# Optimization experiments

Measured on AMD Instinct MI355X. Metric: run time of the kernel, lower is better.

## Reference

```python
import jax, jax.numpy as jnp
import numpy as np

TEMPERATURE = 0.07
EPS = 1e-12


def setup_inputs() -> dict:
    key = jax.random.key(0)
    k1, k2 = jax.random.split(key)
    B, D = 16384, 256
    return {
        "query_embeds": jax.random.normal(k1, (B, D), dtype=jnp.float32),
        "database_embeds": jax.random.normal(k2, (B, D), dtype=jnp.float32),
    }


def _l2_normalize(x, axis=1):
    # torch F.normalize: x / max(||x||, eps)
    norm = jnp.sqrt(jnp.sum(x * x, axis=axis, keepdims=True))
    return x / jnp.maximum(norm, EPS)


def reference(query_embeds, database_embeds):
    q = _l2_normalize(query_embeds, axis=1)   # [B, D]
    d = _l2_normalize(database_embeds, axis=1)  # [B, D]
    sim = jnp.einsum("bd,cd->bc", q, d) / TEMPERATURE  # [B, B]
    B = sim.shape[0]
    diag = jnp.diagonal(sim)  # logits at the correct (matching) label
    # CE over rows (q->d): -log_softmax(sim, axis=1)[i, i]
    lse_rows = jax.nn.logsumexp(sim, axis=1)
    loss_q2d = jnp.mean(lse_rows - diag)
    # CE over rows of sim.T == columns of sim (d->q)
    lse_cols = jax.nn.logsumexp(sim, axis=0)
    loss_d2q = jnp.mean(lse_cols - diag)
    return (loss_q2d + loss_d2q) / 2
```

## Files before the change

kernel.cpp:

```cpp
#include <hip/hip_runtime.h>
#include <hip/hip_bf16.h>
#include <cstdint>
#include <cstddef>

#define B_ROWS 16384
#define D_DIM  256
#define TEMP_INV 14.285714285714286f

#define NITER 16

using frag_cd = __attribute__((ext_vector_type(4))) float;
using i32x4   = __attribute__((ext_vector_type(4))) int;
using i32x8   = __attribute__((ext_vector_type(8))) int;


__global__ __launch_bounds__(256) void norm_diag_kernel(
    const float* __restrict__ q, const float* __restrict__ d,
    unsigned int* __restrict__ qn, unsigned int* __restrict__ dn,
    float* __restrict__ diag,
    float* __restrict__ row_sums, float* __restrict__ col_sums,
    float* __restrict__ out) {
    const int b = blockIdx.x;
    if (b < 64)            row_sums[b * 256 + threadIdx.x] = 0.0f;
    else if (b < 128)      col_sums[(b - 64) * 256 + threadIdx.x] = 0.0f;
    else if (b == 128 && threadIdx.x == 0) out[0] = 0.0f;

    const int t    = threadIdx.x;
    const int lane = t & 63;
    const int w    = t >> 6;
    const int l15  = lane & 15;
    const int rw   = lane >> 4;
    const int r    = w * 4 + rw;
    const int row  = b * 16 + r;

    const float4* qr = (const float4*)(q + (size_t)row * D_DIM);
    const float4* dr = (const float4*)(d + (size_t)row * D_DIM);
    float4 qv[4], dv[4];
    float qss = 0.f, dss = 0.f, qd = 0.f;
#pragma unroll
    for (int p = 0; p < 4; ++p) {
        qv[p] = qr[l15 + 16 * p];
        dv[p] = dr[l15 + 16 * p];
        qss += qv[p].x*qv[p].x + qv[p].y*qv[p].y + qv[p].z*qv[p].z + qv[p].w*qv[p].w;
        dss += dv[p].x*dv[p].x + dv[p].y*dv[p].y + dv[p].z*dv[p].z + dv[p].w*dv[p].w;
        qd  += qv[p].x*dv[p].x + qv[p].y*dv[p].y + qv[p].z*dv[p].z + qv[p].w*dv[p].w;
    }
#pragma unroll
    for (int off = 1; off < 16; off <<= 1) {
        qss += __shfl_xor(qss, off);
        dss += __shfl_xor(dss, off);
        qd  += __shfl_xor(qd,  off);
    }
    const float qinv = 1.0f / fmaxf(sqrtf(qss), 1e-12f);
    const float dinv = 1.0f / fmaxf(sqrtf(dss), 1e-12f);

    __shared__ unsigned int qbuf[1024], dbuf[1024];
#pragma unroll
    for (int p = 0; p < 4; ++p) {
        const int jw = l15 + 16 * p;
        int qp = 0, dp = 0;
        qp = __builtin_amdgcn_cvt_pk_fp8_f32(qv[p].x * qinv, qv[p].y * qinv, qp, false);
        qp = __builtin_amdgcn_cvt_pk_fp8_f32(qv[p].z * qinv, qv[p].w * qinv, qp, true);
        dp = __builtin_amdgcn_cvt_pk_fp8_f32(dv[p].x * dinv, dv[p].y * dinv, dp, false);
        dp = __builtin_amdgcn_cvt_pk_fp8_f32(dv[p].z * dinv, dv[p].w * dinv, dp, true);
        const int c    = (jw & 31) >> 2;
        const int widx = ((jw >> 5) << 9) | ((c >> 2) << 8) | ((c & 3) << 6)
                       | (r << 2) | (jw & 3);
        qbuf[widx] = (unsigned int)qp;
        dbuf[widx] = (unsigned int)dp;
    }
    if (l15 == 0) diag[row] = qd * qinv * dinv * TEMP_INV;
    __syncthreads();
    ((uint4*)qn)[(size_t)b * 256 + t] = ((const uint4*)qbuf)[t];
    ((uint4*)dn)[(size_t)b * 256 + t] = ((const uint4*)dbuf)[t];
}

__global__ __launch_bounds__(256, 2) void gemm_lse_kernel(
    const unsigned char* __restrict__ qn, const unsigned char* __restrict__ dn,
    float* __restrict__ row_sums, float* __restrict__ col_sums) {
    const int t    = threadIdx.x;
    const int lane = t & 63;
    const int w    = t >> 6;
    const int l15  = lane & 15;
    const int quad = lane >> 4;

    const int id   = blockIdx.x;
    const int xcd  = id & 7;
    const int i    = id >> 3;
    const int chunk   = (xcd << 1) | (i & 1);
    const int rowg    = i >> 1;
    const int rowBase = rowg * 256;
    const int colChunkBase = chunk * 1024;

    union OpU { i32x8 v; i32x4 h[2]; };

    const unsigned char* aB = qn + ((size_t)((rowBase >> 4) + w * 4) << 12) + lane * 16;
    OpU a8[4][2];
#pragma unroll
    for (int mi = 0; mi < 4; ++mi)
#pragma unroll
        for (int kt = 0; kt < 2; ++kt) {
            a8[mi][kt].h[0] = *(const i32x4*)(aB + mi * 4096 + kt * 2048);
            a8[mi][kt].h[1] = *(const i32x4*)(aB + mi * 4096 + kt * 2048 + 1024);
        }

    const unsigned char* bBase = dn + ((size_t)(colChunkBase >> 4) << 12) + lane * 16;

    OpU bC[4], bN[4];
#pragma unroll
    for (int ni = 0; ni < 4; ++ni) {
        bC[ni].h[0] = *(const i32x4*)(bBase + ni * 4096);
        bC[ni].h[1] = *(const i32x4*)(bBase + ni * 4096 + 1024);
    }

    union RV { frag_cd v[4]; float f[16]; } rvu;
#pragma unroll
    for (int k = 0; k < 4; ++k) rvu.v[k] = (frag_cd){0.f, 0.f, 0.f, 0.f};

    const float C2 = TEMP_INV * 1.44269504088896f;

    for (int it = 0; it < NITER; ++it) {
        const unsigned char* bI = bBase + (size_t)it * 16384;

#pragma unroll
        for (int ni = 0; ni < 4; ++ni) {
            bN[ni].h[0] = *(const i32x4*)(bI + ni * 4096 + 2048);
            bN[ni].h[1] = *(const i32x4*)(bI + ni * 4096 + 2048 + 1024);
        }

        frag_cd acc[4][4];
#pragma unroll
        for (int mi = 0; mi < 4; ++mi)
#pragma unroll
            for (int ni = 0; ni < 4; ++ni)
                acc[mi][ni] = (frag_cd){0.f, 0.f, 0.f, 0.f};

#pragma unroll
        for (int mi = 0; mi < 4; ++mi)
#pragma unroll
            for (int ni = 0; ni < 4; ++ni)
                acc[mi][ni] = __builtin_amdgcn_mfma_scale_f32_16x16x128_f8f6f4(
                    a8[mi][0].v, bC[ni].v, acc[mi][ni],
                    0, 0, 0, 0x7F7F7F7F, 0, 0x7F7F7F7F);

        if (it != NITER - 1) {
            const unsigned char* bI2 = bI + 16384;
#pragma unroll
            for (int ni = 0; ni < 4; ++ni) {
                bC[ni].h[0] = *(const i32x4*)(bI2 + ni * 4096);
                bC[ni].h[1] = *(const i32x4*)(bI2 + ni * 4096 + 1024);
            }
        }

#pragma unroll
        for (int mi = 0; mi < 4; ++mi)
#pragma unroll
            for (int ni = 0; ni < 4; ++ni)
                acc[mi][ni] = __builtin_amdgcn_mfma_scale_f32_16x16x128_f8f6f4(
                    a8[mi][1].v, bN[ni].v, acc[mi][ni],
                    0, 0, 0, 0x7F7F7F7F, 0, 0x7F7F7F7F);

        frag_cd cv4[4];
#pragma unroll
        for (int k = 0; k < 4; ++k) cv4[k] = (frag_cd){0.f, 0.f, 0.f, 0.f};
#pragma unroll
        for (int mi = 0; mi < 4; ++mi)
#pragma unroll
            for (int ni = 0; ni < 4; ++ni) {
                const frag_cd tt = acc[mi][ni] * C2 - C2;
                frag_cd e;
#pragma unroll
                for (int rr = 0; rr < 4; ++rr) e[rr] = __builtin_amdgcn_exp2f(tt[rr]);
                rvu.v[mi] += e;
                cv4[ni]   += e;
            }
        float cv[4];
#pragma unroll
        for (int ni = 0; ni < 4; ++ni)
            cv[ni] = (cv4[ni][0] + cv4[ni][1]) + (cv4[ni][2] + cv4[ni][3]);

#pragma unroll
        for (int s = 0; s < 2; ++s) {
            const bool bb = (quad >> s) & 1;
#pragma unroll
            for (int k = 0; k < (2 >> s); ++k) {
                const float a0 = cv[2 * k], a1 = cv[2 * k + 1];
                const float keep = bb ? a1 : a0;
                const float send = bb ? a0 : a1;
                cv[k] = keep + __shfl_xor(send, 16 << s);
            }
        }
        atomicAdd(&col_sums[colChunkBase + it * 64 + quad * 16 + l15], cv[0]);
    }

#pragma unroll
    for (int s = 0; s < 4; ++s) {
        const bool bb = (l15 >> s) & 1;
#pragma unroll
        for (int k = 0; k < (8 >> s); ++k) {
            const float a0 = rvu.f[2 * k], a1 = rvu.f[2 * k + 1];
            const float keep = bb ? a1 : a0;
            const float send = bb ? a0 : a1;
            rvu.f[k] = keep + __shfl_xor(send, 1 << s);
        }
    }
    atomicAdd(&row_sums[rowBase + w * 64 + (l15 >> 2) * 16 + quad * 4 + (l15 & 3)],
              rvu.f[0]);
}

__global__ __launch_bounds__(256) void finalize_kernel(
    const float* __restrict__ rs, const float* __restrict__ cs,
    const float* __restrict__ dg, float* __restrict__ out) {
    const int i = blockIdx.x * 256 + threadIdx.x;
    float s = logf(rs[i]) + logf(cs[i]) - 2.0f * dg[i];
#pragma unroll
    for (int off = 32; off; off >>= 1) s += __shfl_down(s, off);
    __shared__ float buf[4];
    if ((threadIdx.x & 63) == 0) buf[threadIdx.x >> 6] = s;
    __syncthreads();
    if (threadIdx.x == 0) {
        float tot = (buf[0] + buf[1] + buf[2] + buf[3]) / (2.0f * B_ROWS);
        if (blockIdx.x == 0) tot += TEMP_INV;
        atomicAdd(out, tot);
    }
}

extern "C" void kernel_launch(void* const* d_in, const int* in_sizes, int n_in,
                              void* d_out, int out_size, void* d_ws, size_t ws_size,
                              hipStream_t stream) {
    const float* q = (const float*)d_in[0];
    const float* d = (const float*)d_in[1];
    float* out = (float*)d_out;

    char* ws = (char*)d_ws;
    unsigned char* qn = (unsigned char*)ws;
    unsigned char* dn = qn + (size_t)B_ROWS * D_DIM;
    float* row_sums = (float*)(ws + 2 * (size_t)B_ROWS * D_DIM);
    float* col_sums = row_sums + B_ROWS;
    float* diag     = col_sums + B_ROWS;

    norm_diag_kernel<<<B_ROWS / 16, 256, 0, stream>>>(
        q, d, (unsigned int*)qn, (unsigned int*)dn, diag, row_sums, col_sums, out);
    gemm_lse_kernel<<<(B_ROWS / 256) * (B_ROWS / 1024), 256, 0, stream>>>(
        qn, dn, row_sums, col_sums);
    finalize_kernel<<<B_ROWS / 256, 256, 0, stream>>>(row_sums, col_sums, diag, out);
}
```

Baseline: 163.6 us.

## Stage B tiles through triple-buffered LDS via async global-to-LDS loads

Before, every wave loaded the B operand tiles straight from global memory into registers. Now the workgroup cooperatively copies each B tile into a three-slot LDS ring with global_load_lds, prefetching two iterations ahead, and each wave reads its fragments from LDS. The aim is to remove the duplicate per-wave global loads of B and to hide load latency behind the MFMA work. It also raises wave priority around the MFMA blocks. The cost is a workgroup barrier every iteration and 48KB of LDS per block, which may limit occupancy under the two-blocks-per-CU launch bound.

```diff
diff --git a/kernel.cpp b/kernel.cpp
--- a/kernel.cpp
+++ b/kernel.cpp
@@ -12,6 +12,13 @@
 using frag_cd = __attribute__((ext_vector_type(4))) float;
 using i32x4   = __attribute__((ext_vector_type(4))) int;
 using i32x8   = __attribute__((ext_vector_type(8))) int;
+
+__device__ __forceinline__ void gld_lds16(const void* g, void* l) {
+    __builtin_amdgcn_global_load_lds(
+        (const __attribute__((address_space(1))) void*)g,
+        (__attribute__((address_space(3))) void*)l,
+        16, 0, 0);
+}
 
 
 __global__ __launch_bounds__(256) void norm_diag_kernel(
@@ -78,6 +85,8 @@
 __global__ __launch_bounds__(256, 2) void gemm_lse_kernel(
     const unsigned char* __restrict__ qn, const unsigned char* __restrict__ dn,
     float* __restrict__ row_sums, float* __restrict__ col_sums) {
+    __shared__ unsigned char ldsB[3][16384];
+
     const int t    = threadIdx.x;
     const int lane = t & 63;
     const int w    = t >> 6;
@@ -104,14 +113,19 @@
             a8[mi][kt].h[1] = *(const i32x4*)(aB + mi * 4096 + kt * 2048 + 1024);
         }
 
-    const unsigned char* bBase = dn + ((size_t)(colChunkBase >> 4) << 12) + lane * 16;
-
-    OpU bC[4], bN[4];
-#pragma unroll
-    for (int ni = 0; ni < 4; ++ni) {
-        bC[ni].h[0] = *(const i32x4*)(bBase + ni * 4096);
-        bC[ni].h[1] = *(const i32x4*)(bBase + ni * 4096 + 1024);
-    }
+    const unsigned char* bG = dn + ((size_t)(colChunkBase >> 4) << 12);
+
+#define STAGE(bufidx, j)                                                      \
+    {                                                                          \
+        const unsigned char* gsrc = bG + (size_t)(j) * 16384;                  \
+        unsigned char* ldst = &ldsB[bufidx][0];                                \
+        _Pragma("unroll")                                                      \
+        for (int ii = 0; ii < 4; ++ii)                                         \
+            gld_lds16(gsrc + ii * 4096 + t * 16, ldst + ii * 4096 + t * 16);   \
+    }
+
+    STAGE(0, 0)
+    STAGE(1, 1)
 
     union RV { frag_cd v[4]; float f[16]; } rvu;
 #pragma unroll
@@ -119,14 +133,18 @@
 
     const float C2 = TEMP_INV * 1.44269504088896f;
 
+    int cur = 0;
+#pragma unroll 1
     for (int it = 0; it < NITER; ++it) {
-        const unsigned char* bI = bBase + (size_t)it * 16384;
-
-#pragma unroll
-        for (int ni = 0; ni < 4; ++ni) {
-            bN[ni].h[0] = *(const i32x4*)(bI + ni * 4096 + 2048);
-            bN[ni].h[1] = *(const i32x4*)(bI + ni * 4096 + 2048 + 1024);
-        }
+        if (it == NITER - 1) asm volatile("s_waitcnt vmcnt(0)" ::: "memory");
+        else                 asm volatile("s_waitcnt vmcnt(4)" ::: "memory");
+        __builtin_amdgcn_s_barrier();
+        asm volatile("" ::: "memory");
+
+        const int nxt = (cur + 2 >= 3) ? cur - 1 : cur + 2;
+        if (it + 2 < NITER) STAGE(nxt, it + 2)
+
+        const unsigned char* bL = &ldsB[cur][0] + lane * 16;
 
         frag_cd acc[4][4];
 #pragma unroll
@@ -135,30 +153,40 @@
             for (int ni = 0; ni < 4; ++ni)
                 acc[mi][ni] = (frag_cd){0.f, 0.f, 0.f, 0.f};
 
-#pragma unroll
-        for (int mi = 0; mi < 4; ++mi)
-#pragma unroll
-            for (int ni = 0; ni < 4; ++ni)
-                acc[mi][ni] = __builtin_amdgcn_mfma_scale_f32_16x16x128_f8f6f4(
-                    a8[mi][0].v, bC[ni].v, acc[mi][ni],
-                    0, 0, 0, 0x7F7F7F7F, 0, 0x7F7F7F7F);
-
-        if (it != NITER - 1) {
-            const unsigned char* bI2 = bI + 16384;
+        {
+            OpU b8[4];
 #pragma unroll
             for (int ni = 0; ni < 4; ++ni) {
-                bC[ni].h[0] = *(const i32x4*)(bI2 + ni * 4096);
-                bC[ni].h[1] = *(const i32x4*)(bI2 + ni * 4096 + 1024);
-            }
-        }
-
-#pragma unroll
-        for (int mi = 0; mi < 4; ++mi)
-#pragma unroll
-            for (int ni = 0; ni < 4; ++ni)
-                acc[mi][ni] = __builtin_amdgcn_mfma_scale_f32_16x16x128_f8f6f4(
-                    a8[mi][1].v, bN[ni].v, acc[mi][ni],
-                    0, 0, 0, 0x7F7F7F7F, 0, 0x7F7F7F7F);
+                b8[ni].h[0] = *(const i32x4*)(bL + ni * 4096);
+                b8[ni].h[1] = *(const i32x4*)(bL + ni * 4096 + 1024);
+            }
+            __builtin_amdgcn_s_setprio(1);
+#pragma unroll
+            for (int mi = 0; mi < 4; ++mi)
+#pragma unroll
+                for (int ni = 0; ni < 4; ++ni)
+                    acc[mi][ni] = __builtin_amdgcn_mfma_scale_f32_16x16x128_f8f6f4(
+                        a8[mi][0].v, b8[ni].v, acc[mi][ni],
+                        0, 0, 0, 0x7F7F7F7F, 0, 0x7F7F7F7F);
+            __builtin_amdgcn_s_setprio(0);
+        }
+        {
+            OpU b8[4];
+#pragma unroll
+            for (int ni = 0; ni < 4; ++ni) {
+                b8[ni].h[0] = *(const i32x4*)(bL + ni * 4096 + 2048);
+                b8[ni].h[1] = *(const i32x4*)(bL + ni * 4096 + 2048 + 1024);
+            }
+            __builtin_amdgcn_s_setprio(1);
+#pragma unroll
+            for (int mi = 0; mi < 4; ++mi)
+#pragma unroll
+                for (int ni = 0; ni < 4; ++ni)
+                    acc[mi][ni] = __builtin_amdgcn_mfma_scale_f32_16x16x128_f8f6f4(
+                        a8[mi][1].v, b8[ni].v, acc[mi][ni],
+                        0, 0, 0, 0x7F7F7F7F, 0, 0x7F7F7F7F);
+            __builtin_amdgcn_s_setprio(0);
+        }
 
         frag_cd cv4[4];
 #pragma unroll
@@ -191,7 +219,10 @@
             }
         }
         atomicAdd(&col_sums[colChunkBase + it * 64 + quad * 16 + l15], cv[0]);
-    }
+
+        cur = (cur + 1 >= 3) ? 0 : cur + 1;
+    }
+#undef STAGE
 
 #pragma unroll
     for (int s = 0; s < 4; ++s) {
```

Result: faster. 149.8 us (-8.5%).

## Restructure GEMM-LSE into single-wave blocks with 64x16 tiles and triple-buffered B loads

Applied to the files above, without the earlier changes.

Blocks shrink from four waves to one wave. Each wave now handles a 64-row strip and walks 1024 columns in 16-column steps instead of 64-column steps, which cuts the accumulator register footprint from 16 fragments to 4. B operands are rotated through a three-deep register buffer so loads run ahead of the MFMAs, and s_setprio raises wave priority during the matrix ops. The intent is higher occupancy and better latency hiding. The cost is four times as many column atomics, since each block now covers a quarter of the rows, and less A-operand reuse per B load.

```diff
diff --git a/kernel.cpp b/kernel.cpp
--- a/kernel.cpp
+++ b/kernel.cpp
@@ -7,7 +7,7 @@
 #define D_DIM  256
 #define TEMP_INV 14.285714285714286f
 
-#define NITER 16
+#define NITER 64
 
 using frag_cd = __attribute__((ext_vector_type(4))) float;
 using i32x4   = __attribute__((ext_vector_type(4))) int;
@@ -75,26 +75,24 @@
     ((uint4*)dn)[(size_t)b * 256 + t] = ((const uint4*)dbuf)[t];
 }
 
-__global__ __launch_bounds__(256, 2) void gemm_lse_kernel(
+__global__ __launch_bounds__(64, 3) void gemm_lse_kernel(
     const unsigned char* __restrict__ qn, const unsigned char* __restrict__ dn,
     float* __restrict__ row_sums, float* __restrict__ col_sums) {
-    const int t    = threadIdx.x;
-    const int lane = t & 63;
-    const int w    = t >> 6;
+    const int lane = threadIdx.x;
     const int l15  = lane & 15;
     const int quad = lane >> 4;
 
-    const int id   = blockIdx.x;
-    const int xcd  = id & 7;
-    const int i    = id >> 3;
-    const int chunk   = (xcd << 1) | (i & 1);
-    const int rowg    = i >> 1;
-    const int rowBase = rowg * 256;
+    const int id    = blockIdx.x;
+    const int xcd   = id & 7;
+    const int i     = id >> 3;
+    const int chunk = (xcd << 1) | (i & 1);
+    const int strip = i >> 1;
+    const int rowBase = strip * 64;
     const int colChunkBase = chunk * 1024;
 
     union OpU { i32x8 v; i32x4 h[2]; };
 
-    const unsigned char* aB = qn + ((size_t)((rowBase >> 4) + w * 4) << 12) + lane * 16;
+    const unsigned char* aB = qn + (size_t)strip * 16384 + lane * 16;
     OpU a8[4][2];
 #pragma unroll
     for (int mi = 0; mi < 4; ++mi)
@@ -104,94 +102,73 @@
             a8[mi][kt].h[1] = *(const i32x4*)(aB + mi * 4096 + kt * 2048 + 1024);
         }
 
-    const unsigned char* bBase = dn + ((size_t)(colChunkBase >> 4) << 12) + lane * 16;
-
-    OpU bC[4], bN[4];
-#pragma unroll
-    for (int ni = 0; ni < 4; ++ni) {
-        bC[ni].h[0] = *(const i32x4*)(bBase + ni * 4096);
-        bC[ni].h[1] = *(const i32x4*)(bBase + ni * 4096 + 1024);
-    }
+    const unsigned char* bG = dn + ((size_t)(colChunkBase >> 4) << 12) + lane * 16;
+
+    OpU b0k0, b0k1, b1k0, b1k1, b2k0, b2k1;
+
+#define LOADB(BK0, BK1, j)                                                    \
+    if ((j) < NITER) {                                                         \
+        const unsigned char* p_ = bG + (size_t)(j) * 4096;                     \
+        BK0.h[0] = *(const i32x4*)(p_);                                        \
+        BK0.h[1] = *(const i32x4*)(p_ + 1024);                                 \
+        BK1.h[0] = *(const i32x4*)(p_ + 2048);                                 \
+        BK1.h[1] = *(const i32x4*)(p_ + 3072);                                 \
+    }
+
+    const float C2 = TEMP_INV * 1.44269504088896f;
+    const frag_cd zf = (frag_cd){0.f, 0.f, 0.f, 0.f};
 
     union RV { frag_cd v[4]; float f[16]; } rvu;
 #pragma unroll
     for (int k = 0; k < 4; ++k) rvu.v[k] = (frag_cd){0.f, 0.f, 0.f, 0.f};
 
-    const float C2 = TEMP_INV * 1.44269504088896f;
-
-    for (int it = 0; it < NITER; ++it) {
-        const unsigned char* bI = bBase + (size_t)it * 16384;
-
-#pragma unroll
-        for (int ni = 0; ni < 4; ++ni) {
-            bN[ni].h[0] = *(const i32x4*)(bI + ni * 4096 + 2048);
-            bN[ni].h[1] = *(const i32x4*)(bI + ni * 4096 + 2048 + 1024);
-        }
-
-        frag_cd acc[4][4];
-#pragma unroll
-        for (int mi = 0; mi < 4; ++mi)
-#pragma unroll
-            for (int ni = 0; ni < 4; ++ni)
-                acc[mi][ni] = (frag_cd){0.f, 0.f, 0.f, 0.f};
-
-#pragma unroll
-        for (int mi = 0; mi < 4; ++mi)
-#pragma unroll
-            for (int ni = 0; ni < 4; ++ni)
-                acc[mi][ni] = __builtin_amdgcn_mfma_scale_f32_16x16x128_f8f6f4(
-                    a8[mi][0].v, bC[ni].v, acc[mi][ni],
-                    0, 0, 0, 0x7F7F7F7F, 0, 0x7F7F7F7F);
-
-        if (it != NITER - 1) {
-            const unsigned char* bI2 = bI + 16384;
-#pragma unroll
-            for (int ni = 0; ni < 4; ++ni) {
-                bC[ni].h[0] = *(const i32x4*)(bI2 + ni * 4096);
-                bC[ni].h[1] = *(const i32x4*)(bI2 + ni * 4096 + 1024);
-            }
-        }
-
-#pragma unroll
-        for (int mi = 0; mi < 4; ++mi)
-#pragma unroll
-            for (int ni = 0; ni < 4; ++ni)
-                acc[mi][ni] = __builtin_amdgcn_mfma_scale_f32_16x16x128_f8f6f4(
-                    a8[mi][1].v, bN[ni].v, acc[mi][ni],
-                    0, 0, 0, 0x7F7F7F7F, 0, 0x7F7F7F7F);
-
-        frag_cd cv4[4];
-#pragma unroll
-        for (int k = 0; k < 4; ++k) cv4[k] = (frag_cd){0.f, 0.f, 0.f, 0.f};
-#pragma unroll
-        for (int mi = 0; mi < 4; ++mi)
-#pragma unroll
-            for (int ni = 0; ni < 4; ++ni) {
-                const frag_cd tt = acc[mi][ni] * C2 - C2;
-                frag_cd e;
-#pragma unroll
-                for (int rr = 0; rr < 4; ++rr) e[rr] = __builtin_amdgcn_exp2f(tt[rr]);
-                rvu.v[mi] += e;
-                cv4[ni]   += e;
-            }
-        float cv[4];
-#pragma unroll
-        for (int ni = 0; ni < 4; ++ni)
-            cv[ni] = (cv4[ni][0] + cv4[ni][1]) + (cv4[ni][2] + cv4[ni][3]);
-
-#pragma unroll
-        for (int s = 0; s < 2; ++s) {
-            const bool bb = (quad >> s) & 1;
-#pragma unroll
-            for (int k = 0; k < (2 >> s); ++k) {
-                const float a0 = cv[2 * k], a1 = cv[2 * k + 1];
-                const float keep = bb ? a1 : a0;
-                const float send = bb ? a0 : a1;
-                cv[k] = keep + __shfl_xor(send, 16 << s);
-            }
-        }
-        atomicAdd(&col_sums[colChunkBase + it * 64 + quad * 16 + l15], cv[0]);
-    }
+#define BODY(BK0, BK1, it)                                                    \
+    {                                                                          \
+        frag_cd acc[4];                                                        \
+        __builtin_amdgcn_s_setprio(1);                                         \
+        _Pragma("unroll")                                                      \
+        for (int mi = 0; mi < 4; ++mi)                                         \
+            acc[mi] = __builtin_amdgcn_mfma_scale_f32_16x16x128_f8f6f4(        \
+                a8[mi][0].v, BK0.v, zf, 0, 0, 0, 0x7F7F7F7F, 0, 0x7F7F7F7F);   \
+        _Pragma("unroll")                                                      \
+        for (int mi = 0; mi < 4; ++mi)                                         \
+            acc[mi] = __builtin_amdgcn_mfma_scale_f32_16x16x128_f8f6f4(        \
+                a8[mi][1].v, BK1.v, acc[mi], 0, 0, 0, 0x7F7F7F7F, 0,           \
+                0x7F7F7F7F);                                                   \
+        __builtin_amdgcn_s_setprio(0);                                         \
+        float cv = 0.f;                                                        \
+        _Pragma("unroll")                                                      \
+        for (int mi = 0; mi < 4; ++mi) {                                       \
+            const frag_cd tt = acc[mi] * C2 - C2;                              \
+            frag_cd e;                                                         \
+            _Pragma("unroll")                                                  \
+            for (int rr = 0; rr < 4; ++rr)                                     \
+                e[rr] = __builtin_amdgcn_exp2f(tt[rr]);                        \
+            rvu.v[mi] += e;                                                    \
+            cv += (e[0] + e[1]) + (e[2] + e[3]);                               \
+        }                                                                      \
+        cv += __shfl_xor(cv, 16);                                              \
+        cv += __shfl_xor(cv, 32);                                              \
+        if (quad == 0)                                                         \
+            atomicAdd(&col_sums[colChunkBase + (it) * 16 + l15], cv);          \
+    }
+
+    LOADB(b0k0, b0k1, 0)
+    LOADB(b1k0, b1k1, 1)
+
+#pragma unroll 1
+    for (int base = 0; base < NITER - 1; base += 3) {
+        LOADB(b2k0, b2k1, base + 2)
+        BODY(b0k0, b0k1, base)
+        LOADB(b0k0, b0k1, base + 3)
+        BODY(b1k0, b1k1, base + 1)
+        LOADB(b1k0, b1k1, base + 4)
+        BODY(b2k0, b2k1, base + 2)
+    }
+    BODY(b0k0, b0k1, NITER - 1)
+
+#undef LOADB
+#undef BODY
 
 #pragma unroll
     for (int s = 0; s < 4; ++s) {
@@ -204,7 +181,7 @@
             rvu.f[k] = keep + __shfl_xor(send, 1 << s);
         }
     }
-    atomicAdd(&row_sums[rowBase + w * 64 + (l15 >> 2) * 16 + quad * 4 + (l15 & 3)],
+    atomicAdd(&row_sums[rowBase + (l15 >> 2) * 16 + quad * 4 + (l15 & 3)],
               rvu.f[0]);
 }
 
@@ -241,7 +218,7 @@
 
     norm_diag_kernel<<<B_ROWS / 16, 256, 0, stream>>>(
         q, d, (unsigned int*)qn, (unsigned int*)dn, diag, row_sums, col_sums, out);
-    gemm_lse_kernel<<<(B_ROWS / 256) * (B_ROWS / 1024), 256, 0, stream>>>(
+    gemm_lse_kernel<<<(B_ROWS / 64) * (B_ROWS / 1024), 64, 0, stream>>>(
         qn, dn, row_sums, col_sums);
     finalize_kernel<<<B_ROWS / 256, 256, 0, stream>>>(row_sums, col_sums, diag, out);
 }
```

After: 342.1 us. 2.09x slower.
